# Kernel optimization log

Hardware: AMD Instinct MI355X
Metric: run time of the kernel (lower is better)

The kernel has to match this reference:

```python
import jax, jax.numpy as jnp
import numpy as np

N = 50000   # nodes
E = 500000  # edges (before self-loops)
D = 256     # out_dim
H = 8       # heads
HD = D // H # head dim
NEG = 0.2   # leaky relu slope (both GAT attention and module act)


def setup_inputs() -> dict:
    key = jax.random.key(0)
    ks = jax.random.split(key, 16)
    s = 0.05
    feats = jax.random.normal(ks[0], (N, D), jnp.float32)
    src = jax.random.randint(ks[1], (E,), 0, N, jnp.int32)
    dst = jax.random.randint(ks[2], (E,), 0, N, jnp.int32)
    proj_W = jax.random.normal(ks[3], (D, D), jnp.float32) * s
    proj_b = jnp.zeros((D,), jnp.float32)
    W1 = jax.random.normal(ks[4], (D, D), jnp.float32) * s
    al1 = jax.random.normal(ks[5], (H, HD), jnp.float32) * s
    ar1 = jax.random.normal(ks[6], (H, HD), jnp.float32) * s
    b1 = jnp.zeros((D,), jnp.float32)
    W2 = jax.random.normal(ks[7], (D, D), jnp.float32) * s
    al2 = jax.random.normal(ks[8], (H, HD), jnp.float32) * s
    ar2 = jax.random.normal(ks[9], (H, HD), jnp.float32) * s
    b2 = jnp.zeros((D,), jnp.float32)
    return dict(feats=feats, src=src, dst=dst, proj_W=proj_W, proj_b=proj_b,
                W1=W1, al1=al1, ar1=ar1, b1=b1, W2=W2, al2=al2, ar2=ar2, b2=b2)


def gat_layer(x, W, al, ar, b, src, dst):
    # x: [N, D] -> h: [N, H, HD]
    h = (x @ W).reshape(N, H, HD)
    el = jnp.einsum('nhd,hd->nh', h, al)   # [N, H]
    er = jnp.einsum('nhd,hd->nh', h, ar)
    e = jax.nn.leaky_relu(el[src] + er[dst], NEG)  # [E+N, H]
    # edge softmax over destination neighborhoods
    m = jax.ops.segment_max(e, dst, num_segments=N)       # [N, H]
    a = jnp.exp(e - m[dst])
    z = jax.ops.segment_sum(a, dst, num_segments=N)       # [N, H]
    alpha = a / z[dst]                                     # [E+N, H]
    out = jax.ops.segment_sum(alpha[:, :, None] * h[src], dst, num_segments=N)  # [N,H,HD]
    out = out + b.reshape(H, HD)
    return out.reshape(N, D)


def reference(feats, src, dst, proj_W, proj_b, W1, al1, ar1, b1, W2, al2, ar2, b2):
    # dgl.add_self_loop
    loop = jnp.arange(N, dtype=src.dtype)
    s = jnp.concatenate([src, loop])
    d = jnp.concatenate([dst, loop])
    x = feats @ proj_W + proj_b
    for W, al, ar, b in ((W1, al1, ar1, b1), (W2, al2, ar2, b2)):
        x = gat_layer(x, W, al, ar, b, s, d)
        x = jax.nn.leaky_relu(x, NEG)  # module act; dropout = eval no-op
    return x
```

## Files before the change

### kernel.cpp

```cpp
#include <hip/hip_runtime.h>
#include <stdint.h>
#include <stddef.h>

#define NNODES 50000
#define NEDGES 500000
#define DIM 256
#define NHEAD 8
#define HDIM 32
#define MPAD 50048
#define NEGS 0.2f
#define SCAN_BLOCKS 196
#define COUNT_BLOCKS 1954
#define CVT_BLOCKS 12500
#define TR_BLOCKS 192
#define GEMM_BLOCKS 782

typedef __attribute__((ext_vector_type(8))) short bf16x8;
typedef __attribute__((ext_vector_type(4))) float f32x4;
typedef __attribute__((ext_vector_type(4))) unsigned short u16x4;

__device__ __forceinline__ unsigned short f2bf(float f) {
    uint32_t u = __builtin_bit_cast(uint32_t, f);
    uint32_t r = (u + 0x7FFFu + ((u >> 16) & 1u)) >> 16;
    return (unsigned short)r;
}

__device__ __forceinline__ float bf2f(unsigned short u) {
    return __builtin_bit_cast(float, (uint32_t)u << 16);
}

__device__ __forceinline__ float bf2f_s(short u) {
    return __builtin_bit_cast(float, (uint32_t)(unsigned short)u << 16);
}

__device__ __forceinline__ float leaky(float x) {
    return x > 0.0f ? x : NEGS * x;
}

__device__ __forceinline__ void gld_lds16(const unsigned short* g, unsigned short* l) {
    __builtin_amdgcn_global_load_lds(
        (const __attribute__((address_space(1))) void*)g,
        (__attribute__((address_space(3))) void*)l,
        16, 0, 0);
}


__global__ __launch_bounds__(256) void scanA_kernel(const int* __restrict__ deg,
                                                    int* __restrict__ bsum) {
    __shared__ int ws[4];
    int t = threadIdx.x;
    int idx = blockIdx.x * 256 + t;
    int v = (idx < NNODES) ? deg[idx] : 0;
    int x = v;
    #pragma unroll
    for (int off = 1; off < 64; off <<= 1) x += __shfl_xor(x, off, 64);
    if ((t & 63) == 0) ws[t >> 6] = x;
    __syncthreads();
    if (t == 0) bsum[blockIdx.x] = ws[0] + ws[1] + ws[2] + ws[3];
}

__global__ __launch_bounds__(256) void scanB_kernel(const int* __restrict__ bsum,
                                                    int* __restrict__ boff,
                                                    int* __restrict__ rowptr) {
    __shared__ int s[256];
    int t = threadIdx.x;
    int v = (t < SCAN_BLOCKS) ? bsum[t] : 0;
    s[t] = v;
    __syncthreads();
    #pragma unroll
    for (int off = 1; off < 256; off <<= 1) {
        int y = (t >= off) ? s[t - off] : 0;
        __syncthreads();
        s[t] += y;
        __syncthreads();
    }
    if (t < SCAN_BLOCKS) boff[t] = s[t] - v;
    if (t == 0) rowptr[NNODES] = NEDGES;
}

__global__ __launch_bounds__(256) void scanC_kernel(const int* __restrict__ deg,
                                                    const int* __restrict__ boff,
                                                    int* __restrict__ rowptr,
                                                    int* __restrict__ cursor) {
    __shared__ int ws[4];
    int t = threadIdx.x;
    int lane = t & 63, wv = t >> 6;
    int idx = blockIdx.x * 256 + t;
    int v = (idx < NNODES) ? deg[idx] : 0;
    int x = v;
    #pragma unroll
    for (int off = 1; off < 64; off <<= 1) {
        int y = __shfl_up(x, off, 64);
        if (lane >= off) x += y;
    }
    if (lane == 63) ws[wv] = x;
    __syncthreads();
    int wadd = 0;
    #pragma unroll
    for (int k = 0; k < 4; ++k) if (k < wv) wadd += ws[k];
    int excl = x - v + wadd + boff[blockIdx.x];
    if (idx < NNODES) { rowptr[idx] = excl; cursor[idx] = excl; }
}


__global__ __launch_bounds__(256) void combo1(const int* __restrict__ dst,
                                              int* __restrict__ deg,
                                              const float* __restrict__ feats,
                                              unsigned short* __restrict__ Abf,
                                              const float* __restrict__ W0,
                                              const float* __restrict__ W1,
                                              const float* __restrict__ W2,
                                              unsigned short* __restrict__ WT) {
    __shared__ float tile[32][33];
    int b = blockIdx.x;
    if (b < COUNT_BLOCKS) {
        int i = b * 256 + threadIdx.x;
        if (i < NEDGES) atomicAdd(&deg[dst[i]], 1);
    } else if (b < COUNT_BLOCKS + CVT_BLOCKS) {
        int i = ((b - COUNT_BLOCKS) * 256 + threadIdx.x) * 4;
        const float4 v = *(const float4*)(feats + i);
        u16x4 o;
        o.x = f2bf(v.x); o.y = f2bf(v.y); o.z = f2bf(v.z); o.w = f2bf(v.w);
        *(u16x4*)(Abf + i) = o;
    } else {
        int t = b - COUNT_BLOCKS - CVT_BLOCKS;
        int bz = t >> 6;
        int bx = t & 7;
        int by = (t >> 3) & 7;
        const float* W = (bz == 0) ? W0 : (bz == 1) ? W1 : W2;
        unsigned short* T = WT + (size_t)bz * DIM * DIM;
        int tx = threadIdx.x & 31, ty = threadIdx.x >> 5;
        #pragma unroll
        for (int j = 0; j < 4; ++j)
            tile[ty + j * 8][tx] = W[(by * 32 + ty + j * 8) * DIM + bx * 32 + tx];
        __syncthreads();
        #pragma unroll
        for (int j = 0; j < 4; ++j)
            T[(bx * 32 + ty + j * 8) * DIM + by * 32 + tx] = f2bf(tile[tx][ty + j * 8]);
    }
}


__device__ __forceinline__ void gemm_body(int bx, int by,
        const unsigned short* __restrict__ A, const unsigned short* __restrict__ BT,
        unsigned short* __restrict__ Cb, const float* __restrict__ bias) {
    __shared__ __align__(16) unsigned short As[4][128][32];
    __shared__ __align__(16) unsigned short Bs[4][128][32];
    int tid = threadIdx.x;
    int wave = tid >> 6, lane = tid & 63;
    int row0 = bx * 128;
    int col0 = by * 128;
    int wm = (wave >> 1) * 64;
    int wn = (wave & 1) * 64;

    f32x4 acc[4][4] = {};

    int fr = lane & 15;
    int kg = (lane >> 4) * 8;

    #pragma unroll
    for (int half = 0; half < 2; ++half) {
        int k0 = half * 128;
        #pragma unroll
        for (int r = 0; r < 8; ++r) {
            int idx = r * 256 + tid;
            int c = idx >> 9;
            int rem = idx & 511;
            int row = rem >> 2;
            int q = rem & 3;
            gld_lds16(A + (size_t)(row0 + row) * DIM + k0 + c * 32 + q * 8,
                      &As[0][0][0] + idx * 8);
            gld_lds16(BT + (size_t)(col0 + row) * DIM + k0 + c * 32 + q * 8,
                      &Bs[0][0][0] + idx * 8);
        }
        __syncthreads();

        #pragma unroll
        for (int c = 0; c < 4; ++c) {
            bf16x8 a_frag[4], b_frag[4];
            #pragma unroll
            for (int i = 0; i < 4; ++i) {
                a_frag[i] = *(const bf16x8*)(&As[c][wm + i * 16 + fr][kg]);
                b_frag[i] = *(const bf16x8*)(&Bs[c][wn + i * 16 + fr][kg]);
            }
            #pragma unroll
            for (int i = 0; i < 4; ++i)
                #pragma unroll
                for (int j = 0; j < 4; ++j)
                    acc[i][j] = __builtin_amdgcn_mfma_f32_16x16x32_bf16(
                        a_frag[i], b_frag[j], acc[i][j], 0, 0, 0);
        }
        __syncthreads();
    }

    int rg = (lane >> 4) * 4;
    #pragma unroll
    for (int i = 0; i < 4; ++i) {
        #pragma unroll
        for (int j = 0; j < 4; ++j) {
            int n = col0 + wn + j * 16 + fr;
            float bv = bias ? bias[n] : 0.0f;
            #pragma unroll
            for (int r = 0; r < 4; ++r) {
                int m = row0 + wm + i * 16 + rg + r;
                Cb[(size_t)m * DIM + n] = f2bf(acc[i][j][r] + bv);
            }
        }
    }
}

__global__ __launch_bounds__(256) void gemm_kernel(const unsigned short* __restrict__ A,
                                                   const unsigned short* __restrict__ BT,
                                                   unsigned short* __restrict__ Cb,
                                                   const float* __restrict__ bias) {
    gemm_body(blockIdx.x, blockIdx.y, A, BT, Cb, bias);
}


__global__ __launch_bounds__(256) void combo2(const unsigned short* __restrict__ A,
                                              const unsigned short* __restrict__ BT,
                                              unsigned short* __restrict__ Cb,
                                              const float* __restrict__ bias,
                                              const int* __restrict__ src,
                                              const int* __restrict__ dst,
                                              int* __restrict__ cursor,
                                              int* __restrict__ csr) {
    int b = blockIdx.x;
    if (b < GEMM_BLOCKS) {
        gemm_body(b % 391, b / 391, A, BT, Cb, bias);
    } else {
        int i = (b - GEMM_BLOCKS) * 256 + threadIdx.x;
        if (i < NEDGES) {
            int pos = atomicAdd(&cursor[dst[i]], 1);
            csr[pos] = src[i];
        }
    }
}


__global__ __launch_bounds__(256) void eler_kernel(const unsigned short* __restrict__ Hb,
                                                   const float* __restrict__ al,
                                                   const float* __restrict__ ar,
                                                   float* __restrict__ el,
                                                   float* __restrict__ er) {
    int wave = threadIdx.x >> 6;
    int lane = threadIdx.x & 63;
    int v = blockIdx.x * 4 + wave;
    if (v >= NNODES) return;
    int c0 = lane * 4;
    ushort4 h = *(const ushort4*)(Hb + (size_t)v * DIM + c0);
    float4 a = *(const float4*)(al + c0);
    float4 r = *(const float4*)(ar + c0);
    float h0 = bf2f(h.x), h1 = bf2f(h.y), h2 = bf2f(h.z), h3 = bf2f(h.w);
    float x = h0 * a.x + h1 * a.y + h2 * a.z + h3 * a.w;
    float y = h0 * r.x + h1 * r.y + h2 * r.z + h3 * r.w;
    #pragma unroll
    for (int off = 1; off < 8; off <<= 1) {
        x += __shfl_xor(x, off, 64);
        y += __shfl_xor(y, off, 64);
    }
    if ((lane & 7) == 0) {
        int head = lane >> 3;
        el[v * NHEAD + head] = x;
        er[v * NHEAD + head] = y;
    }
}


__global__ __launch_bounds__(256) void agg_kernel(const unsigned short* __restrict__ Hb,
                                                  const float* __restrict__ el,
                                                  const float* __restrict__ er,
                                                  const int* __restrict__ rowptr,
                                                  const int* __restrict__ csr,
                                                  const float* __restrict__ bias,
                                                  float* __restrict__ outf,
                                                  unsigned short* __restrict__ outb) {
    int wave = threadIdx.x >> 6;
    int lane = threadIdx.x & 63;
    int v = blockIdx.x * 4 + wave;
    if (v >= NNODES) return;
    int sub = lane & 31;
    int halfe = lane >> 5;
    int c0 = sub * 8;
    int head = sub >> 2;

    float er_v = er[v * NHEAD + head];
    float el_v = el[v * NHEAD + head];
    int beg = rowptr[v], end = rowptr[v + 1];

    float z = 0.0f;
    float acc[8] = {0.f, 0.f, 0.f, 0.f, 0.f, 0.f, 0.f, 0.f};

    if (halfe == 0) {
        float ws = __expf(leaky(el_v + er_v));
        z = ws;
        bf16x8 h = *(const bf16x8*)(Hb + (size_t)v * DIM + c0);
        #pragma unroll
        for (int d = 0; d < 8; ++d) acc[d] = ws * bf2f_s(h[d]);
    }

    #pragma unroll 4
    for (int i = beg + halfe; i < end; i += 2) {
        int u = csr[i];
        float e = leaky(el[u * NHEAD + head] + er_v);
        float wi = __expf(e);
        z += wi;
        bf16x8 h = *(const bf16x8*)(Hb + (size_t)u * DIM + c0);
        #pragma unroll
        for (int d = 0; d < 8; ++d) acc[d] += wi * bf2f_s(h[d]);
    }

    z += __shfl_xor(z, 32, 64);
    #pragma unroll
    for (int d = 0; d < 8; ++d) acc[d] += __shfl_xor(acc[d], 32, 64);

    float inv = 1.0f / z;
    int o0 = c0 + halfe * 4;
    float4 b = *(const float4*)(bias + o0);
    float r0 = leaky(acc[halfe * 4 + 0] * inv + b.x);
    float r1 = leaky(acc[halfe * 4 + 1] * inv + b.y);
    float r2 = leaky(acc[halfe * 4 + 2] * inv + b.z);
    float r3 = leaky(acc[halfe * 4 + 3] * inv + b.w);
    if (outf) {
        float4 o = { r0, r1, r2, r3 };
        *(float4*)(outf + (size_t)v * DIM + o0) = o;
    } else {
        u16x4 o;
        o.x = f2bf(r0); o.y = f2bf(r1); o.z = f2bf(r2); o.w = f2bf(r3);
        *(u16x4*)(outb + (size_t)v * DIM + o0) = o;
    }
}


static inline size_t align256(size_t x) { return (x + 255) & ~(size_t)255; }

extern "C" void kernel_launch(void* const* d_in, const int* in_sizes, int n_in,
                              void* d_out, int out_size, void* d_ws, size_t ws_size,
                              hipStream_t stream) {
    const float* feats  = (const float*)d_in[0];
    const int*   src    = (const int*)d_in[1];
    const int*   dst    = (const int*)d_in[2];
    const float* proj_W = (const float*)d_in[3];
    const float* proj_b = (const float*)d_in[4];
    const float* W1     = (const float*)d_in[5];
    const float* al1    = (const float*)d_in[6];
    const float* ar1    = (const float*)d_in[7];
    const float* b1     = (const float*)d_in[8];
    const float* W2     = (const float*)d_in[9];
    const float* al2    = (const float*)d_in[10];
    const float* ar2    = (const float*)d_in[11];
    const float* b2     = (const float*)d_in[12];
    float* out = (float*)d_out;

    uint8_t* w = (uint8_t*)d_ws;
    unsigned short* Abf = (unsigned short*)w; w += align256((size_t)MPAD * DIM * 2);
    unsigned short* Bbf = (unsigned short*)w; w += align256((size_t)MPAD * DIM * 2);
    unsigned short* Hb  = (unsigned short*)w; w += align256((size_t)MPAD * DIM * 2);
    unsigned short* WT  = (unsigned short*)w; w += align256((size_t)3 * DIM * DIM * 2);
    float* el = (float*)w;            w += align256((size_t)NNODES * NHEAD * 4);
    float* er = (float*)w;            w += align256((size_t)NNODES * NHEAD * 4);
    int* deg    = (int*)w;            w += align256((size_t)NNODES * 4);
    int* rowptr = (int*)w;            w += align256((size_t)(NNODES + 1) * 4);
    int* cursor = (int*)w;            w += align256((size_t)NNODES * 4);
    int* csr    = (int*)w;            w += align256((size_t)NEDGES * 4);
    int* bsum   = (int*)w;            w += align256((size_t)SCAN_BLOCKS * 4);
    int* boff   = (int*)w;            w += align256((size_t)SCAN_BLOCKS * 4);

    unsigned short* WT0 = WT;
    unsigned short* WT1 = WT + (size_t)DIM * DIM;
    unsigned short* WT2 = WT + (size_t)2 * DIM * DIM;

    const dim3 gemm_grid(MPAD / 128, DIM / 128);
    const int node_wave_blocks = (NNODES + 3) / 4;

    hipMemsetAsync(deg, 0, (size_t)NNODES * 4, stream);

    combo1<<<COUNT_BLOCKS + CVT_BLOCKS + TR_BLOCKS, 256, 0, stream>>>(
        dst, deg, feats, Abf, proj_W, W1, W2, WT);

    scanA_kernel<<<SCAN_BLOCKS, 256, 0, stream>>>(deg, bsum);
    scanB_kernel<<<1, 256, 0, stream>>>(bsum, boff, rowptr);
    scanC_kernel<<<SCAN_BLOCKS, 256, 0, stream>>>(deg, boff, rowptr, cursor);

    combo2<<<GEMM_BLOCKS + COUNT_BLOCKS, 256, 0, stream>>>(
        Abf, WT0, Bbf, proj_b, src, dst, cursor, csr);

    gemm_kernel<<<gemm_grid, 256, 0, stream>>>(Bbf, WT1, Hb, nullptr);
    eler_kernel<<<node_wave_blocks, 256, 0, stream>>>(Hb, al1, ar1, el, er);
    agg_kernel<<<node_wave_blocks, 256, 0, stream>>>(Hb, el, er, rowptr, csr, b1,
                                                     nullptr, Abf);

    gemm_kernel<<<gemm_grid, 256, 0, stream>>>(Abf, WT2, Hb, nullptr);
    eler_kernel<<<node_wave_blocks, 256, 0, stream>>>(Hb, al2, ar2, el, er);
    agg_kernel<<<node_wave_blocks, 256, 0, stream>>>(Hb, el, er, rowptr, csr, b2,
                                                     out, nullptr);
}
```

Measured before the change: 340.0 us.

## Restructure GAT aggregation to four edge slots with packed bf16 math

```diff
diff --git a/kernel.cpp b/kernel.cpp
--- a/kernel.cpp
+++ b/kernel.cpp
@@ -17,6 +17,7 @@
 
 typedef __attribute__((ext_vector_type(8))) short bf16x8;
 typedef __attribute__((ext_vector_type(4))) float f32x4;
+typedef __attribute__((ext_vector_type(2))) float f32x2;
 typedef __attribute__((ext_vector_type(4))) unsigned short u16x4;
 
 __device__ __forceinline__ unsigned short f2bf(float f) {
@@ -29,8 +30,11 @@
     return __builtin_bit_cast(float, (uint32_t)u << 16);
 }
 
-__device__ __forceinline__ float bf2f_s(short u) {
-    return __builtin_bit_cast(float, (uint32_t)(unsigned short)u << 16);
+__device__ __forceinline__ f32x2 bfpair(uint32_t w) {
+    f32x2 r;
+    r.x = __builtin_bit_cast(float, w << 16);
+    r.y = __builtin_bit_cast(float, w & 0xffff0000u);
+    return r;
 }
 
 __device__ __forceinline__ float leaky(float x) {
@@ -267,6 +271,27 @@
 }
 
 
+__device__ __forceinline__ void edge_acc(const unsigned short* __restrict__ Hb,
+                                         const float* __restrict__ el,
+                                         int u, int head, float er_v, int c0,
+                                         float& z, f32x2 (&acc2)[8]) {
+    float e = leaky(el[u * NHEAD + head] + er_v);
+    float wi = __expf(e);
+    z += wi;
+    const unsigned short* hp = Hb + (size_t)u * DIM + c0;
+    uint4 h0 = *(const uint4*)(hp);
+    uint4 h1 = *(const uint4*)(hp + 8);
+    f32x2 w2 = {wi, wi};
+    acc2[0] += w2 * bfpair(h0.x);
+    acc2[1] += w2 * bfpair(h0.y);
+    acc2[2] += w2 * bfpair(h0.z);
+    acc2[3] += w2 * bfpair(h0.w);
+    acc2[4] += w2 * bfpair(h1.x);
+    acc2[5] += w2 * bfpair(h1.y);
+    acc2[6] += w2 * bfpair(h1.z);
+    acc2[7] += w2 * bfpair(h1.w);
+}
+
 __global__ __launch_bounds__(256) void agg_kernel(const unsigned short* __restrict__ Hb,
                                                   const float* __restrict__ el,
                                                   const float* __restrict__ er,
@@ -279,50 +304,77 @@
     int lane = threadIdx.x & 63;
     int v = blockIdx.x * 4 + wave;
     if (v >= NNODES) return;
-    int sub = lane & 31;
-    int halfe = lane >> 5;
-    int c0 = sub * 8;
-    int head = sub >> 2;
+    int q = lane >> 4;
+    int s16 = lane & 15;
+    int c0 = s16 * 16;
+    int head = s16 >> 1;
 
     float er_v = er[v * NHEAD + head];
     float el_v = el[v * NHEAD + head];
     int beg = rowptr[v], end = rowptr[v + 1];
+    int deg = end - beg;
 
     float z = 0.0f;
-    float acc[8] = {0.f, 0.f, 0.f, 0.f, 0.f, 0.f, 0.f, 0.f};
-
-    if (halfe == 0) {
+    f32x2 acc2[8] = {};
+
+    if (q == 0) {
         float ws = __expf(leaky(el_v + er_v));
         z = ws;
-        bf16x8 h = *(const bf16x8*)(Hb + (size_t)v * DIM + c0);
-        #pragma unroll
-        for (int d = 0; d < 8; ++d) acc[d] = ws * bf2f_s(h[d]);
-    }
-
-    #pragma unroll 4
-    for (int i = beg + halfe; i < end; i += 2) {
-        int u = csr[i];
-        float e = leaky(el[u * NHEAD + head] + er_v);
-        float wi = __expf(e);
-        z += wi;
-        bf16x8 h = *(const bf16x8*)(Hb + (size_t)u * DIM + c0);
-        #pragma unroll
-        for (int d = 0; d < 8; ++d) acc[d] += wi * bf2f_s(h[d]);
-    }
-
+        const unsigned short* hp = Hb + (size_t)v * DIM + c0;
+        uint4 h0 = *(const uint4*)(hp);
+        uint4 h1 = *(const uint4*)(hp + 8);
+        f32x2 w2 = {ws, ws};
+        acc2[0] = w2 * bfpair(h0.x);
+        acc2[1] = w2 * bfpair(h0.y);
+        acc2[2] = w2 * bfpair(h0.z);
+        acc2[3] = w2 * bfpair(h0.w);
+        acc2[4] = w2 * bfpair(h1.x);
+        acc2[5] = w2 * bfpair(h1.y);
+        acc2[6] = w2 * bfpair(h1.z);
+        acc2[7] = w2 * bfpair(h1.w);
+    }
+
+    if (deg <= 64) {
+        int myu = (lane < deg) ? csr[beg + lane] : 0;
+        int nt = (deg + 3) >> 2;
+        #pragma unroll 2
+        for (int t = 0; t < nt; ++t) {
+            int k = 4 * t + q;
+            int u = __shfl(myu, k, 64);
+            if (k < deg)
+                edge_acc(Hb, el, u, head, er_v, c0, z, acc2);
+        }
+    } else {
+        for (int k = beg + q; k < end; k += 4) {
+            int u = csr[k];
+            edge_acc(Hb, el, u, head, er_v, c0, z, acc2);
+        }
+    }
+
+    z += __shfl_xor(z, 16, 64);
     z += __shfl_xor(z, 32, 64);
     #pragma unroll
-    for (int d = 0; d < 8; ++d) acc[d] += __shfl_xor(acc[d], 32, 64);
+    for (int j = 0; j < 8; ++j) {
+        acc2[j].x += __shfl_xor(acc2[j].x, 16, 64);
+        acc2[j].y += __shfl_xor(acc2[j].y, 16, 64);
+        acc2[j].x += __shfl_xor(acc2[j].x, 32, 64);
+        acc2[j].y += __shfl_xor(acc2[j].y, 32, 64);
+    }
 
     float inv = 1.0f / z;
-    int o0 = c0 + halfe * 4;
+    f32x2 pa, pb;
+    if (q == 0)      { pa = acc2[0]; pb = acc2[1]; }
+    else if (q == 1) { pa = acc2[2]; pb = acc2[3]; }
+    else if (q == 2) { pa = acc2[4]; pb = acc2[5]; }
+    else             { pa = acc2[6]; pb = acc2[7]; }
+    int o0 = c0 + q * 4;
     float4 b = *(const float4*)(bias + o0);
-    float r0 = leaky(acc[halfe * 4 + 0] * inv + b.x);
-    float r1 = leaky(acc[halfe * 4 + 1] * inv + b.y);
-    float r2 = leaky(acc[halfe * 4 + 2] * inv + b.z);
-    float r3 = leaky(acc[halfe * 4 + 3] * inv + b.w);
+    float r0 = leaky(pa.x * inv + b.x);
+    float r1 = leaky(pa.y * inv + b.y);
+    float r2 = leaky(pb.x * inv + b.z);
+    float r3 = leaky(pb.y * inv + b.w);
     if (outf) {
-        float4 o = { r0, r1, r2, r3 };
+        float4 o = {r0, r1, r2, r3};
         *(float4*)(outf + (size_t)v * DIM + o0) = o;
     } else {
         u16x4 o;
```

New measurement: 338.5 us. About the same (-0.5%).

## Double-buffer A tiles, read B from global, remap GEMM blocks per XCD

Applied to the files above, without the earlier changes.

```diff
diff --git a/kernel.cpp b/kernel.cpp
--- a/kernel.cpp
+++ b/kernel.cpp
@@ -42,6 +42,13 @@
         (const __attribute__((address_space(1))) void*)g,
         (__attribute__((address_space(3))) void*)l,
         16, 0, 0);
+}
+
+__device__ __forceinline__ void xcd_pair(int orig, int& bx, int& by) {
+    int x = orig & 7, g = orig >> 3;
+    int v = (x < 6 ? x * 98 : 588 + (x - 6) * 97) + g;
+    bx = v >> 1;
+    by = v & 1;
 }
 
 
@@ -144,8 +151,7 @@
 __device__ __forceinline__ void gemm_body(int bx, int by,
         const unsigned short* __restrict__ A, const unsigned short* __restrict__ BT,
         unsigned short* __restrict__ Cb, const float* __restrict__ bias) {
-    __shared__ __align__(16) unsigned short As[4][128][32];
-    __shared__ __align__(16) unsigned short Bs[4][128][32];
+    __shared__ __align__(16) unsigned short As2[2][2][128][32];
     int tid = threadIdx.x;
     int wave = tid >> 6, lane = tid & 63;
     int row0 = bx * 128;
@@ -158,30 +164,37 @@
     int fr = lane & 15;
     int kg = (lane >> 4) * 8;
 
-    #pragma unroll
-    for (int half = 0; half < 2; ++half) {
-        int k0 = half * 128;
-        #pragma unroll
-        for (int r = 0; r < 8; ++r) {
-            int idx = r * 256 + tid;
-            int c = idx >> 9;
-            int rem = idx & 511;
-            int row = rem >> 2;
-            int q = rem & 3;
-            gld_lds16(A + (size_t)(row0 + row) * DIM + k0 + c * 32 + q * 8,
-                      &As[0][0][0] + idx * 8);
-            gld_lds16(BT + (size_t)(col0 + row) * DIM + k0 + c * 32 + q * 8,
-                      &Bs[0][0][0] + idx * 8);
-        }
-        __syncthreads();
-
-        #pragma unroll
-        for (int c = 0; c < 4; ++c) {
+    const unsigned short* Bw = BT + (size_t)(col0 + wn + fr) * DIM + kg;
+
+    #define STAGE(buf, kt)                                                        \
+        do {                                                                      \
+            _Pragma("unroll")                                                     \
+            for (int r_ = 0; r_ < 4; ++r_) {                                      \
+                int idx_ = r_ * 256 + tid;                                        \
+                int c_ = idx_ >> 9;                                               \
+                int rem_ = idx_ & 511;                                            \
+                int row_ = rem_ >> 2;                                             \
+                int q_ = rem_ & 3;                                                \
+                gld_lds16(A + (size_t)(row0 + row_) * DIM + (kt) * 64 + c_ * 32 + q_ * 8, \
+                          &As2[buf][0][0][0] + idx_ * 8);                         \
+            }                                                                     \
+        } while (0)
+
+    STAGE(0, 0);
+    __syncthreads();
+
+    int cur = 0;
+    #pragma unroll
+    for (int t = 0; t < 4; ++t) {
+        if (t < 3) STAGE(cur ^ 1, t + 1);
+        #pragma unroll
+        for (int c = 0; c < 2; ++c) {
+            int kk = t * 64 + c * 32;
             bf16x8 a_frag[4], b_frag[4];
             #pragma unroll
             for (int i = 0; i < 4; ++i) {
-                a_frag[i] = *(const bf16x8*)(&As[c][wm + i * 16 + fr][kg]);
-                b_frag[i] = *(const bf16x8*)(&Bs[c][wn + i * 16 + fr][kg]);
+                a_frag[i] = *(const bf16x8*)(&As2[cur][c][wm + i * 16 + fr][kg]);
+                b_frag[i] = *(const bf16x8*)(Bw + (size_t)i * 16 * DIM + kk);
             }
             #pragma unroll
             for (int i = 0; i < 4; ++i)
@@ -190,8 +203,9 @@
                     acc[i][j] = __builtin_amdgcn_mfma_f32_16x16x32_bf16(
                         a_frag[i], b_frag[j], acc[i][j], 0, 0, 0);
         }
-        __syncthreads();
-    }
+        if (t < 3) { __syncthreads(); cur ^= 1; }
+    }
+    #undef STAGE
 
     int rg = (lane >> 4) * 4;
     #pragma unroll
@@ -213,7 +227,9 @@
                                                    const unsigned short* __restrict__ BT,
                                                    unsigned short* __restrict__ Cb,
                                                    const float* __restrict__ bias) {
-    gemm_body(blockIdx.x, blockIdx.y, A, BT, Cb, bias);
+    int bx, by;
+    xcd_pair(blockIdx.x, bx, by);
+    gemm_body(bx, by, A, BT, Cb, bias);
 }
 
 
@@ -227,7 +243,9 @@
                                               int* __restrict__ csr) {
     int b = blockIdx.x;
     if (b < GEMM_BLOCKS) {
-        gemm_body(b % 391, b / 391, A, BT, Cb, bias);
+        int bx, by;
+        xcd_pair(b, bx, by);
+        gemm_body(bx, by, A, BT, Cb, bias);
     } else {
         int i = (b - GEMM_BLOCKS) * 256 + threadIdx.x;
         if (i < NEDGES) {
@@ -370,7 +388,6 @@
     unsigned short* WT1 = WT + (size_t)DIM * DIM;
     unsigned short* WT2 = WT + (size_t)2 * DIM * DIM;
 
-    const dim3 gemm_grid(MPAD / 128, DIM / 128);
     const int node_wave_blocks = (NNODES + 3) / 4;
 
     hipMemsetAsync(deg, 0, (size_t)NNODES * 4, stream);
@@ -385,12 +402,12 @@
     combo2<<<GEMM_BLOCKS + COUNT_BLOCKS, 256, 0, stream>>>(
         Abf, WT0, Bbf, proj_b, src, dst, cursor, csr);
 
-    gemm_kernel<<<gemm_grid, 256, 0, stream>>>(Bbf, WT1, Hb, nullptr);
+    gemm_kernel<<<GEMM_BLOCKS, 256, 0, stream>>>(Bbf, WT1, Hb, nullptr);
     eler_kernel<<<node_wave_blocks, 256, 0, stream>>>(Hb, al1, ar1, el, er);
     agg_kernel<<<node_wave_blocks, 256, 0, stream>>>(Hb, el, er, rowptr, csr, b1,
                                                      nullptr, Abf);
 
-    gemm_kernel<<<gemm_grid, 256, 0, stream>>>(Abf, WT2, Hb, nullptr);
+    gemm_kernel<<<GEMM_BLOCKS, 256, 0, stream>>>(Abf, WT2, Hb, nullptr);
     eler_kernel<<<node_wave_blocks, 256, 0, stream>>>(Hb, al2, ar2, el, er);
     agg_kernel<<<node_wave_blocks, 256, 0, stream>>>(Hb, el, er, rowptr, csr, b2,
                                                      out, nullptr);
```

Result: slower. 359.5 us (+5.7%).
